# Optimization experiments

Hardware: AMD Instinct MI355X
Metric: run time of the kernel (lower is better)

Reference implementation:

```python
import jax, jax.numpy as jnp
import numpy as np

N_HEADS = 16
KQ_DIM = 64
EMB_DIM = 1024
CTX_DIM = 1024
EPS = 1e-5

def _layernorm(x, w, b):
    # LayerNorm over last dim (kq_dim), elementwise affine
    mu = jnp.mean(x, axis=-1, keepdims=True)
    var = jnp.mean(jnp.square(x - mu), axis=-1, keepdims=True)
    return (x - mu) * jax.lax.rsqrt(var + EPS) * w + b

def setup_inputs() -> dict:
    key = jax.random.key(0)
    ks = jax.random.split(key, 10)
    B, SQ, SK = 2, 2048, 2048
    inner = N_HEADS * KQ_DIM
    s_e = 1.0 / np.sqrt(EMB_DIM)
    s_c = 1.0 / np.sqrt(CTX_DIM)
    s_i = 1.0 / np.sqrt(inner)
    return {
        "emb": jax.random.normal(ks[0], (B, SQ, EMB_DIM), jnp.float32),
        "context": jax.random.normal(ks[1], (B, SK, CTX_DIM), jnp.float32),
        "Wq": jax.random.uniform(ks[2], (inner, EMB_DIM), jnp.float32, -s_e, s_e),
        "Wk": jax.random.uniform(ks[3], (inner, CTX_DIM), jnp.float32, -s_c, s_c),
        "Wv": jax.random.uniform(ks[4], (inner, CTX_DIM), jnp.float32, -s_c, s_c),
        "Wu": jax.random.uniform(ks[5], (EMB_DIM, inner), jnp.float32, -s_i, s_i),
        "bu": jax.random.uniform(ks[6], (EMB_DIM,), jnp.float32, -s_i, s_i),
        "qn_w": jnp.ones((KQ_DIM,), jnp.float32),
        "qn_b": jnp.zeros((KQ_DIM,), jnp.float32),
        "kn_w": jnp.ones((KQ_DIM,), jnp.float32),
        "kn_b": jnp.zeros((KQ_DIM,), jnp.float32),
    }

def reference(emb, context, Wq, Wk, Wv, Wu, bu, qn_w, qn_b, kn_w, kn_b):
    B, SQ, _ = emb.shape
    SK = context.shape[1]
    # projections (no bias), reshape to [B, H, S, D]
    q = (emb @ Wq.T).reshape(B, SQ, N_HEADS, KQ_DIM).transpose(0, 2, 1, 3)
    k = (context @ Wk.T).reshape(B, SK, N_HEADS, KQ_DIM).transpose(0, 2, 1, 3)
    v = (context @ Wv.T).reshape(B, SK, N_HEADS, KQ_DIM).transpose(0, 2, 1, 3)
    q = _layernorm(q, qn_w, qn_b)
    k = _layernorm(k, kn_w, kn_b)
    scale = 1.0 / jnp.sqrt(jnp.asarray(KQ_DIM, emb.dtype))
    attn = jnp.einsum('bhqd,bhkd->bhqk', q, k) * scale
    attn = jax.nn.softmax(attn, axis=-1)
    out = jnp.einsum('bhqk,bhkd->bhqd', attn, v)
    out = out.transpose(0, 2, 1, 3).reshape(B, SQ, N_HEADS * KQ_DIM)
    return out @ Wu.T + bu
```

## Files before the change

kernel.cpp:

```cpp
#include <hip/hip_runtime.h>


typedef __attribute__((ext_vector_type(8)))  short bf16x8;
typedef __attribute__((ext_vector_type(4)))  short bf16x4;
typedef __attribute__((ext_vector_type(4)))  float f32x4;
typedef __attribute__((ext_vector_type(16))) float f32x16;
typedef __attribute__((ext_vector_type(4)))  unsigned int u32x4;

#define SM_SCALE 0.18033688f

typedef __attribute__((address_space(1))) const void cg_void;
typedef __attribute__((address_space(3))) void lds_void_t;

__device__ __forceinline__ void gl_lds16(const void* g, void* l){
  __builtin_amdgcn_global_load_lds((cg_void*)g, (lds_void_t*)l, 16, 0, 0);
}

__device__ __forceinline__ short f2b(float f){
  unsigned int u;
  __builtin_memcpy(&u, &f, 4);
  u += 0x7fffu + ((u >> 16) & 1u);
  return (short)(u >> 16);
}

__global__ __launch_bounds__(256) void cvt6_kernel(
    const float* __restrict__ emb, const float* __restrict__ ctx,
    const float* __restrict__ Wq, const float* __restrict__ Wk,
    const float* __restrict__ Wv, const float* __restrict__ Wu,
    short* __restrict__ o_emb, short* __restrict__ o_ctx,
    short* __restrict__ o_wq, short* __restrict__ o_wk,
    short* __restrict__ o_wv, short* __restrict__ o_wu)
{
  const long M1 = 1024L * 1024L, M4 = 4L * M1;
  long e = ((long)blockIdx.x * 256 + threadIdx.x) * 4;
  if (e >= 12L * M1) return;
  const float* src; short* dst; long off;
  if      (e <     M4)      { src = emb; dst = o_emb; off = e;           }
  else if (e < 2 * M4)      { src = ctx; dst = o_ctx; off = e - M4;      }
  else if (e < 2 * M4 + M1) { src = Wq;  dst = o_wq;  off = e - 2 * M4;  }
  else if (e < 2 * M4 + 2*M1){src = Wk;  dst = o_wk;  off = e - 2*M4 - M1;}
  else if (e < 2 * M4 + 3*M1){src = Wv;  dst = o_wv;  off = e - 2*M4 - 2*M1;}
  else                      { src = Wu;  dst = o_wu;  off = e - 2*M4 - 3*M1;}
  f32x4 v = *(const f32x4*)(src + off);
  bf16x4 o;
  o[0] = f2b(v[0]); o[1] = f2b(v[1]); o[2] = f2b(v[2]); o[3] = f2b(v[3]);
  *(bf16x4*)(dst + off) = o;
}

__global__ __launch_bounds__(256, 3) void gemm_qkv_kernel(
    const short* __restrict__ embh, const short* __restrict__ ctxh,
    const short* __restrict__ Wqh, const short* __restrict__ Wkh,
    const short* __restrict__ Wvh,
    short* __restrict__ qo, short* __restrict__ ko, short* __restrict__ vto,
    const float* __restrict__ qw, const float* __restrict__ qb,
    const float* __restrict__ kw, const float* __restrict__ kb)
{
  const int K = 1024;
  __shared__ short As[128 * 64];
  __shared__ short Bs[128 * 64];
  const int tid  = threadIdx.x;
  const int wave = tid >> 6, lane = tid & 63;
  const int quad = lane >> 4, r16 = lane & 15;
  const int wm = (wave >> 1) * 64, wn = (wave & 1) * 64;

  const int task = blockIdx.y;
  int bn, bm;
  const short *A, *B;
  if (task == 2){
    bn = (blockIdx.x & 31) * 128; bm = (blockIdx.x >> 5) * 128;
    A = Wvh; B = ctxh;
  } else {
    bm = (blockIdx.x & 31) * 128; bn = (blockIdx.x >> 5) * 128;
    A = task ? ctxh : embh; B = task ? Wkh : Wqh;
  }

  f32x4 acc[4][4];
#pragma unroll
  for (int i = 0; i < 4; i++)
#pragma unroll
    for (int j = 0; j < 4; j++)
      acc[i][j] = (f32x4){0.f, 0.f, 0.f, 0.f};

  const int sr7 = (lane >> 3) & 7;
  const size_t arow = (size_t)(bm + wave * 8 + (lane >> 3)) * K
                      + (((lane & 7) ^ sr7) * 8);
  const size_t brow = (size_t)(bn + wave * 8 + (lane >> 3)) * K
                      + (((lane & 7) ^ sr7) * 8);
  const int sw = ((quad ^ (r16 & 7)) << 3);

  for (int k0 = 0; k0 < K; k0 += 64){
#pragma unroll
    for (int i = 0; i < 4; i++)
      gl_lds16(A + arow + (size_t)32 * i * K + k0, &As[wave * 512 + i * 2048]);
#pragma unroll
    for (int i = 0; i < 4; i++)
      gl_lds16(B + brow + (size_t)32 * i * K + k0, &Bs[wave * 512 + i * 2048]);
    __syncthreads();
#pragma unroll
    for (int kk = 0; kk < 2; kk++){
      const int off = sw ^ (kk << 5);
      bf16x8 af[4], bq[4];
#pragma unroll
      for (int i = 0; i < 4; i++)
        af[i] = *(const bf16x8*)(&As[(wm + i*16 + r16) * 64 + off]);
#pragma unroll
      for (int j = 0; j < 4; j++)
        bq[j] = *(const bf16x8*)(&Bs[(wn + j*16 + r16) * 64 + off]);
#pragma unroll
      for (int i = 0; i < 4; i++)
#pragma unroll
        for (int j = 0; j < 4; j++)
          acc[i][j] = __builtin_amdgcn_mfma_f32_16x16x32_bf16(af[i], bq[j], acc[i][j], 0, 0, 0);
    }
    __syncthreads();
  }

  if (task < 2){
    short* Ch = task ? ko : qo;
    const float* lw = task ? kw : qw;
    const float* lb = task ? kb : qb;
    const float post = task ? 1.0f : SM_SCALE;
    float wv[4], bv[4];
#pragma unroll
    for (int j = 0; j < 4; j++){
      wv[j] = lw[j*16 + r16] * post;
      bv[j] = lb[j*16 + r16] * post;
    }
#pragma unroll
    for (int i = 0; i < 4; i++){
#pragma unroll
      for (int t = 0; t < 4; t++){
        float a[4];
#pragma unroll
        for (int j = 0; j < 4; j++) a[j] = acc[i][j][t];
        float s = a[0] + a[1] + a[2] + a[3];
        s += __shfl_xor(s, 1); s += __shfl_xor(s, 2);
        s += __shfl_xor(s, 4); s += __shfl_xor(s, 8);
        const float mu = s * 0.015625f;
        float d[4], sq = 0.f;
#pragma unroll
        for (int j = 0; j < 4; j++){ d[j] = a[j] - mu; sq += d[j]*d[j]; }
        sq += __shfl_xor(sq, 1); sq += __shfl_xor(sq, 2);
        sq += __shfl_xor(sq, 4); sq += __shfl_xor(sq, 8);
        const float si = rsqrtf(sq * 0.015625f + 1e-5f);
        const size_t row = (size_t)(bm + wm + i*16 + quad*4 + t);
#pragma unroll
        for (int j = 0; j < 4; j++)
          Ch[row * 1024 + (bn + wn + j*16 + r16)] = f2b(d[j] * si * wv[j] + bv[j]);
      }
    }
  } else {
#pragma unroll
    for (int i = 0; i < 4; i++){
#pragma unroll
      for (int j4 = 0; j4 < 4; j4++){
#pragma unroll
        for (int t = 0; t < 4; t++){
          const int row  = bm + wm + i*16 + quad*4 + t;
          const int col0 = bn + wn + j4*16 + r16;
          const int bb  = col0 >> 11, tok = col0 & 2047;
          const int hq  = row >> 6,  dd  = row & 63;
          const int mt  = dd >> 5,   q5l = dd & 31;
          const int kt  = tok >> 6,  tk  = tok & 63;
          const int s32 = (tk >> 5) & 1, ks = tk & 31;
          const int hi  = ks >> 4,   r   = ks & 15;
          const int cc  = r >> 3, hh2 = (r >> 2) & 1, jj = (r & 3) + 4*hi;
          const size_t addr = ((size_t)(bb*16 + hq) * 32 + kt) * 4096
                            + (size_t)(((mt*2 + s32)*2 + cc) * 512)
                            + (hh2*32 + q5l) * 8 + jj;
          vto[addr] = f2b(acc[i][j4][t]);
        }
      }
    }
  }
}

__global__ __launch_bounds__(256, 4) void gemm_out_kernel(
    const short* __restrict__ A, const short* __restrict__ B,
    float* __restrict__ Cf, const float* __restrict__ bias)
{
  const int K = 1024, N = 1024;
  __shared__ short As[64 * 64];
  __shared__ short Bs[64 * 64];
  const int tid  = threadIdx.x;
  const int wave = tid >> 6, lane = tid & 63;
  const int quad = lane >> 4, r16 = lane & 15;
  const int wm = (wave >> 1) * 32, wn = (wave & 1) * 32;
  const int bm = blockIdx.x * 64, bn = blockIdx.y * 64;

  f32x4 acc[2][2];
#pragma unroll
  for (int i = 0; i < 2; i++)
#pragma unroll
    for (int j = 0; j < 2; j++)
      acc[i][j] = (f32x4){0.f, 0.f, 0.f, 0.f};

  const int sr7 = (lane >> 3) & 7;
  const size_t arow = (size_t)(bm + wave * 8 + (lane >> 3)) * K
                      + (((lane & 7) ^ sr7) * 8);
  const size_t brow = (size_t)(bn + wave * 8 + (lane >> 3)) * K
                      + (((lane & 7) ^ sr7) * 8);
  const int sw = ((quad ^ (r16 & 7)) << 3);

  for (int k0 = 0; k0 < K; k0 += 64){
#pragma unroll
    for (int i = 0; i < 2; i++){
      gl_lds16(A + arow + (size_t)32 * i * K + k0, &As[wave * 512 + i * 2048]);
      gl_lds16(B + brow + (size_t)32 * i * K + k0, &Bs[wave * 512 + i * 2048]);
    }
    __syncthreads();
#pragma unroll
    for (int kk = 0; kk < 2; kk++){
      const int off = sw ^ (kk << 5);
      bf16x8 af[2], bq[2];
#pragma unroll
      for (int i = 0; i < 2; i++)
        af[i] = *(const bf16x8*)(&As[(wm + i*16 + r16) * 64 + off]);
#pragma unroll
      for (int j = 0; j < 2; j++)
        bq[j] = *(const bf16x8*)(&Bs[(wn + j*16 + r16) * 64 + off]);
#pragma unroll
      for (int i = 0; i < 2; i++)
#pragma unroll
        for (int j = 0; j < 2; j++)
          acc[i][j] = __builtin_amdgcn_mfma_f32_16x16x32_bf16(af[i], bq[j], acc[i][j], 0, 0, 0);
    }
    __syncthreads();
  }

#pragma unroll
  for (int i = 0; i < 2; i++){
#pragma unroll
    for (int j = 0; j < 2; j++){
      const int col = bn + wn + j*16 + r16;
#pragma unroll
      for (int t = 0; t < 4; t++){
        const size_t row = (size_t)(bm + wm + i*16 + quad*4 + t);
        Cf[row * N + col] = acc[i][j][t] + bias[col];
      }
    }
  }
}

__global__ __launch_bounds__(256, 2) void flash2_kernel(
    const short* __restrict__ Q, const short* __restrict__ K,
    const short* __restrict__ Vt, short* __restrict__ O)
{
  __shared__ __align__(16) long long smem8[4096];
  short* Ks = (short*)smem8;
  float* scr = (float*)smem8;

  const int tid = threadIdx.x;
  const int wave = tid >> 6, lane = tid & 63;
  const int half = wave >> 1, wg = wave & 1;
  const int hh = lane >> 5, q5 = lane & 31;
  const int h = blockIdx.x, qb = blockIdx.y, b = blockIdx.z;
  const int q0 = qb * 128 + wg * 64;

  const size_t kbase = ((size_t)b * 2048) * 1024 + (size_t)h * 64;
  const short* vbh = Vt + ((size_t)(b * 16 + h)) * 131072;

  bf16x8 qf[2][4];
#pragma unroll
  for (int qg = 0; qg < 2; qg++){
    const size_t qrow = ((size_t)b * 2048 + q0 + qg * 32 + q5) * 1024 + (size_t)h * 64;
#pragma unroll
    for (int c = 0; c < 4; c++)
      qf[qg][c] = *(const bf16x8*)(Q + qrow + c * 16 + hh * 8);
  }

  f32x16 oacc[2][2];
#pragma unroll
  for (int t = 0; t < 16; t++){
    oacc[0][0][t] = 0.f; oacc[0][1][t] = 0.f;
    oacc[1][0][t] = 0.f; oacc[1][1][t] = 0.f;
  }
  float lacc[2] = {0.f, 0.f};

  const int srow = lane >> 3;
  const int csrc = ((lane & 7) ^ srow) * 8;
  const int wr0 = wg * 32;

#define STAGE(bufi, kt)                                                         \
  {                                                                             \
    const short* ks = K + kbase + (size_t)((kt) * 64 + wr0 + srow) * 1024 + csrc; \
    short* kd = Ks + (half * 2 + (bufi)) * 4096 + wr0 * 64;                     \
    gl_lds16(ks,             kd);                                               \
    gl_lds16(ks +  8 * 1024, kd + 512);                                         \
    gl_lds16(ks + 16 * 1024, kd + 1024);                                        \
    gl_lds16(ks + 24 * 1024, kd + 1536);                                        \
  }

  STAGE(0, half)

  for (int i = 0; i < 16; i++){
    const int buf = i & 1;
    __syncthreads();
    if (i + 1 < 16) STAGE(buf ^ 1, 2 * (i + 1) + half)

    const int ktc = 2 * i + half;

    bf16x8 vfr[2][2][2];
#pragma unroll
    for (int s32 = 0; s32 < 2; s32++)
#pragma unroll
      for (int c = 0; c < 2; c++)
#pragma unroll
        for (int mt = 0; mt < 2; mt++)
          vfr[s32][c][mt] = *(const bf16x8*)(
              vbh + (size_t)ktc * 4096 + (((mt*2 + s32)*2 + c) * 512) + lane * 8);

    const short* kb_l = Ks + (half * 2 + buf) * 4096;

    bf16x8 kf[2][4];
#pragma unroll
    for (int s32 = 0; s32 < 2; s32++){
      const int key = s32 * 32 + q5;
#pragma unroll
      for (int c = 0; c < 4; c++)
        kf[s32][c] = *(const bf16x8*)(&kb_l[key * 64 + (((2*c + hh) ^ (key & 7)) << 3)]);
    }

    f32x16 sacc[2][2];
#pragma unroll
    for (int t = 0; t < 16; t++){
      sacc[0][0][t] = 0.f; sacc[0][1][t] = 0.f;
      sacc[1][0][t] = 0.f; sacc[1][1][t] = 0.f;
    }
#pragma unroll
    for (int c = 0; c < 4; c++){
      sacc[0][0] = __builtin_amdgcn_mfma_f32_32x32x16_bf16(kf[0][c], qf[0][c], sacc[0][0], 0, 0, 0);
      sacc[0][1] = __builtin_amdgcn_mfma_f32_32x32x16_bf16(kf[1][c], qf[0][c], sacc[0][1], 0, 0, 0);
      sacc[1][0] = __builtin_amdgcn_mfma_f32_32x32x16_bf16(kf[0][c], qf[1][c], sacc[1][0], 0, 0, 0);
      sacc[1][1] = __builtin_amdgcn_mfma_f32_32x32x16_bf16(kf[1][c], qf[1][c], sacc[1][1], 0, 0, 0);
    }

    bf16x8 pf[2][2][2];
#pragma unroll
    for (int qg = 0; qg < 2; qg++){
#pragma unroll
      for (int s32 = 0; s32 < 2; s32++){
        unsigned int pu[16];
        float pp[4] = {0.f, 0.f, 0.f, 0.f};
#pragma unroll
        for (int t = 0; t < 16; t++){
          const float e = __builtin_amdgcn_exp2f(sacc[qg][s32][t]);
          pp[t & 3] += e;
          unsigned int u; __builtin_memcpy(&u, &e, 4);
          pu[t] = u + 0x8000u;
        }
        lacc[qg] += (pp[0] + pp[1]) + (pp[2] + pp[3]);
#pragma unroll
        for (int c = 0; c < 2; c++){
          u32x4 tmp;
          tmp[0] = __builtin_amdgcn_perm(pu[4*c + 1], pu[4*c + 0], 0x07060302u);
          tmp[1] = __builtin_amdgcn_perm(pu[4*c + 3], pu[4*c + 2], 0x07060302u);
          tmp[2] = __builtin_amdgcn_perm(pu[8 + 4*c + 1], pu[8 + 4*c + 0], 0x07060302u);
          tmp[3] = __builtin_amdgcn_perm(pu[8 + 4*c + 3], pu[8 + 4*c + 2], 0x07060302u);
          __builtin_memcpy(&pf[qg][s32][c], &tmp, 16);
        }
      }
    }

#pragma unroll
    for (int s32 = 0; s32 < 2; s32++){
#pragma unroll
      for (int c = 0; c < 2; c++){
#pragma unroll
        for (int mt = 0; mt < 2; mt++){
          oacc[0][mt] = __builtin_amdgcn_mfma_f32_32x32x16_bf16(vfr[s32][c][mt], pf[0][s32][c], oacc[0][mt], 0, 0, 0);
          oacc[1][mt] = __builtin_amdgcn_mfma_f32_32x32x16_bf16(vfr[s32][c][mt], pf[1][s32][c], oacc[1][mt], 0, 0, 0);
        }
      }
    }
  }

  const int widx = wg * 64 + lane;
  __syncthreads();
#pragma unroll
  for (int qg = 0; qg < 2; qg++){
    const float lh = lacc[qg] + __shfl_xor(lacc[qg], 32);
    if (half == 1){
      float* base = scr + widx * 33;
#pragma unroll
      for (int t = 0; t < 16; t++){ base[t] = oacc[qg][0][t]; base[16 + t] = oacc[qg][1][t]; }
      scr[4224 + widx] = lh;
    }
    __syncthreads();
    if (half == 0){
      const float* base = scr + widx * 33;
      const float l2 = scr[4224 + widx];
      const float linv = 1.0f / (lh + l2);
      const size_t orow = ((size_t)b * 2048 + q0 + qg * 32 + q5) * 1024 + (size_t)h * 64;
#pragma unroll
      for (int mt = 0; mt < 2; mt++){
#pragma unroll
        for (int g = 0; g < 4; g++){
          bf16x4 o4;
#pragma unroll
          for (int u = 0; u < 4; u++)
            o4[u] = f2b((oacc[qg][mt][g*4 + u] + base[mt*16 + g*4 + u]) * linv);
          *(bf16x4*)(O + orow + mt*32 + g*8 + 4*hh) = o4;
        }
      }
    }
    __syncthreads();
  }
}
#undef STAGE

extern "C" void kernel_launch(void* const* d_in, const int* in_sizes, int n_in,
                              void* d_out, int out_size, void* d_ws, size_t ws_size,
                              hipStream_t stream) {
  const float* emb  = (const float*)d_in[0];
  const float* ctx  = (const float*)d_in[1];
  const float* Wq   = (const float*)d_in[2];
  const float* Wk   = (const float*)d_in[3];
  const float* Wv   = (const float*)d_in[4];
  const float* Wu   = (const float*)d_in[5];
  const float* bu   = (const float*)d_in[6];
  const float* qn_w = (const float*)d_in[7];
  const float* qn_b = (const float*)d_in[8];
  const float* kn_w = (const float*)d_in[9];
  const float* kn_b = (const float*)d_in[10];
  float* out = (float*)d_out;

  const size_t BIG = (size_t)4096 * 1024;
  const size_t WSZ = (size_t)1024 * 1024;
  short* ws   = (short*)d_ws;
  short* embh = ws;
  short* ctxh = embh + BIG;
  short* Wqh  = ctxh + BIG;
  short* Wkh  = Wqh + WSZ;
  short* Wvh  = Wkh + WSZ;
  short* Wuh  = Wvh + WSZ;
  short* qh   = Wuh + WSZ;
  short* kh   = qh + BIG;
  short* vth  = kh + BIG;
  short* aoh  = vth + BIG;

  cvt6_kernel<<<12288, 256, 0, stream>>>(emb, ctx, Wq, Wk, Wv, Wu,
                                         embh, ctxh, Wqh, Wkh, Wvh, Wuh);

  gemm_qkv_kernel<<<dim3(256, 3), 256, 0, stream>>>(
      embh, ctxh, Wqh, Wkh, Wvh, qh, kh, vth,
      qn_w, qn_b, kn_w, kn_b);

  flash2_kernel<<<dim3(16, 16, 2), 256, 0, stream>>>(qh, kh, vth, aoh);

  gemm_out_kernel<<<dim3(64, 16), 256, 0, stream>>>(aoh, Wuh, out, bu);
}
```

Baseline: 190.4 us.

## Pre-swizzle K into MFMA fragment layout and load directly to registers

```diff
diff --git a/kernel.cpp b/kernel.cpp
--- a/kernel.cpp
+++ b/kernel.cpp
@@ -116,7 +116,6 @@
   }
 
   if (task < 2){
-    short* Ch = task ? ko : qo;
     const float* lw = task ? kw : qw;
     const float* lb = task ? kb : qb;
     const float post = task ? 1.0f : SM_SCALE;
@@ -143,10 +142,27 @@
         sq += __shfl_xor(sq, 1); sq += __shfl_xor(sq, 2);
         sq += __shfl_xor(sq, 4); sq += __shfl_xor(sq, 8);
         const float si = rsqrtf(sq * 0.015625f + 1e-5f);
-        const size_t row = (size_t)(bm + wm + i*16 + quad*4 + t);
-#pragma unroll
-        for (int j = 0; j < 4; j++)
-          Ch[row * 1024 + (bn + wn + j*16 + r16)] = f2b(d[j] * si * wv[j] + bv[j]);
+        const int row = bm + wm + i*16 + quad*4 + t;
+        if (task == 0){
+#pragma unroll
+          for (int j = 0; j < 4; j++)
+            qo[(size_t)row * 1024 + (bn + wn + j*16 + r16)] =
+                f2b(d[j] * si * wv[j] + bv[j]);
+        } else {
+          const int bb = row >> 11, key = row & 2047;
+          const int kt = key >> 6, tk = key & 63;
+          const int s32 = tk >> 5, q5k = tk & 31;
+#pragma unroll
+          for (int j = 0; j < 4; j++){
+            const int col = bn + wn + j*16 + r16;
+            const int hq = col >> 6, dd = col & 63;
+            const int cc = dd >> 4, hh2 = (dd >> 3) & 1, jj = dd & 7;
+            const size_t addr = ((size_t)(bb*16 + hq) * 32 + kt) * 4096
+                              + (size_t)((s32*4 + cc) * 512)
+                              + (hh2*32 + q5k) * 8 + jj;
+            ko[addr] = f2b(d[j] * si * wv[j] + bv[j]);
+          }
+        }
       }
     }
   } else {
@@ -243,12 +259,10 @@
 }
 
 __global__ __launch_bounds__(256, 2) void flash2_kernel(
-    const short* __restrict__ Q, const short* __restrict__ K,
+    const short* __restrict__ Q, const short* __restrict__ Kf,
     const short* __restrict__ Vt, short* __restrict__ O)
 {
-  __shared__ __align__(16) long long smem8[4096];
-  short* Ks = (short*)smem8;
-  float* scr = (float*)smem8;
+  __shared__ __align__(16) float scr[4352];
 
   const int tid = threadIdx.x;
   const int wave = tid >> 6, lane = tid & 63;
@@ -257,7 +271,7 @@
   const int h = blockIdx.x, qb = blockIdx.y, b = blockIdx.z;
   const int q0 = qb * 128 + wg * 64;
 
-  const size_t kbase = ((size_t)b * 2048) * 1024 + (size_t)h * 64;
+  const short* kbh = Kf + ((size_t)(b * 16 + h)) * 131072;
   const short* vbh = Vt + ((size_t)(b * 16 + h)) * 131072;
 
   bf16x8 qf[2][4];
@@ -277,103 +291,91 @@
   }
   float lacc[2] = {0.f, 0.f};
 
-  const int srow = lane >> 3;
-  const int csrc = ((lane & 7) ^ srow) * 8;
-  const int wr0 = wg * 32;
-
-#define STAGE(bufi, kt)                                                         \
-  {                                                                             \
-    const short* ks = K + kbase + (size_t)((kt) * 64 + wr0 + srow) * 1024 + csrc; \
-    short* kd = Ks + (half * 2 + (bufi)) * 4096 + wr0 * 64;                     \
-    gl_lds16(ks,             kd);                                               \
-    gl_lds16(ks +  8 * 1024, kd + 512);                                         \
-    gl_lds16(ks + 16 * 1024, kd + 1024);                                        \
-    gl_lds16(ks + 24 * 1024, kd + 1536);                                        \
-  }
-
-  STAGE(0, half)
-
-  for (int i = 0; i < 16; i++){
-    const int buf = i & 1;
-    __syncthreads();
-    if (i + 1 < 16) STAGE(buf ^ 1, 2 * (i + 1) + half)
-
-    const int ktc = 2 * i + half;
-
-    bf16x8 vfr[2][2][2];
-#pragma unroll
-    for (int s32 = 0; s32 < 2; s32++)
-#pragma unroll
-      for (int c = 0; c < 2; c++)
-#pragma unroll
-        for (int mt = 0; mt < 2; mt++)
-          vfr[s32][c][mt] = *(const bf16x8*)(
-              vbh + (size_t)ktc * 4096 + (((mt*2 + s32)*2 + c) * 512) + lane * 8);
-
-    const short* kb_l = Ks + (half * 2 + buf) * 4096;
-
-    bf16x8 kf[2][4];
-#pragma unroll
-    for (int s32 = 0; s32 < 2; s32++){
-      const int key = s32 * 32 + q5;
-#pragma unroll
-      for (int c = 0; c < 4; c++)
-        kf[s32][c] = *(const bf16x8*)(&kb_l[key * 64 + (((2*c + hh) ^ (key & 7)) << 3)]);
-    }
-
-    f32x16 sacc[2][2];
-#pragma unroll
-    for (int t = 0; t < 16; t++){
-      sacc[0][0][t] = 0.f; sacc[0][1][t] = 0.f;
-      sacc[1][0][t] = 0.f; sacc[1][1][t] = 0.f;
-    }
-#pragma unroll
-    for (int c = 0; c < 4; c++){
-      sacc[0][0] = __builtin_amdgcn_mfma_f32_32x32x16_bf16(kf[0][c], qf[0][c], sacc[0][0], 0, 0, 0);
-      sacc[0][1] = __builtin_amdgcn_mfma_f32_32x32x16_bf16(kf[1][c], qf[0][c], sacc[0][1], 0, 0, 0);
-      sacc[1][0] = __builtin_amdgcn_mfma_f32_32x32x16_bf16(kf[0][c], qf[1][c], sacc[1][0], 0, 0, 0);
-      sacc[1][1] = __builtin_amdgcn_mfma_f32_32x32x16_bf16(kf[1][c], qf[1][c], sacc[1][1], 0, 0, 0);
-    }
-
-    bf16x8 pf[2][2][2];
-#pragma unroll
-    for (int qg = 0; qg < 2; qg++){
-#pragma unroll
-      for (int s32 = 0; s32 < 2; s32++){
-        unsigned int pu[16];
-        float pp[4] = {0.f, 0.f, 0.f, 0.f};
-#pragma unroll
-        for (int t = 0; t < 16; t++){
-          const float e = __builtin_amdgcn_exp2f(sacc[qg][s32][t]);
-          pp[t & 3] += e;
-          unsigned int u; __builtin_memcpy(&u, &e, 4);
-          pu[t] = u + 0x8000u;
-        }
-        lacc[qg] += (pp[0] + pp[1]) + (pp[2] + pp[3]);
-#pragma unroll
-        for (int c = 0; c < 2; c++){
-          u32x4 tmp;
-          tmp[0] = __builtin_amdgcn_perm(pu[4*c + 1], pu[4*c + 0], 0x07060302u);
-          tmp[1] = __builtin_amdgcn_perm(pu[4*c + 3], pu[4*c + 2], 0x07060302u);
-          tmp[2] = __builtin_amdgcn_perm(pu[8 + 4*c + 1], pu[8 + 4*c + 0], 0x07060302u);
-          tmp[3] = __builtin_amdgcn_perm(pu[8 + 4*c + 3], pu[8 + 4*c + 2], 0x07060302u);
-          __builtin_memcpy(&pf[qg][s32][c], &tmp, 16);
-        }
-      }
-    }
-
-#pragma unroll
-    for (int s32 = 0; s32 < 2; s32++){
-#pragma unroll
-      for (int c = 0; c < 2; c++){
-#pragma unroll
-        for (int mt = 0; mt < 2; mt++){
-          oacc[0][mt] = __builtin_amdgcn_mfma_f32_32x32x16_bf16(vfr[s32][c][mt], pf[0][s32][c], oacc[0][mt], 0, 0, 0);
-          oacc[1][mt] = __builtin_amdgcn_mfma_f32_32x32x16_bf16(vfr[s32][c][mt], pf[1][s32][c], oacc[1][mt], 0, 0, 0);
-        }
-      }
-    }
-  }
+#define LOADK(dst, ktc)                                                      \
+  {                                                                          \
+    const short* kp = kbh + (size_t)(ktc) * 4096 + lane * 8;                 \
+    _Pragma("unroll")                                                        \
+    for (int s32 = 0; s32 < 2; s32++)                                        \
+      _Pragma("unroll")                                                      \
+      for (int c = 0; c < 4; c++)                                            \
+        dst[s32][c] = *(const bf16x8*)(kp + (s32*4 + c) * 512);              \
+  }
+
+#define BODY(kfX, ktc)                                                       \
+  {                                                                          \
+    bf16x8 vfr[2][2][2];                                                     \
+    _Pragma("unroll")                                                        \
+    for (int s32 = 0; s32 < 2; s32++)                                        \
+      _Pragma("unroll")                                                      \
+      for (int c = 0; c < 2; c++)                                            \
+        _Pragma("unroll")                                                    \
+        for (int mt = 0; mt < 2; mt++)                                       \
+          vfr[s32][c][mt] = *(const bf16x8*)(                                \
+              vbh + (size_t)(ktc) * 4096 + (((mt*2 + s32)*2 + c) * 512) + lane * 8); \
+    f32x16 sacc[2][2];                                                       \
+    _Pragma("unroll")                                                        \
+    for (int t = 0; t < 16; t++){                                            \
+      sacc[0][0][t] = 0.f; sacc[0][1][t] = 0.f;                              \
+      sacc[1][0][t] = 0.f; sacc[1][1][t] = 0.f;                              \
+    }                                                                        \
+    _Pragma("unroll")                                                        \
+    for (int c = 0; c < 4; c++){                                             \
+      sacc[0][0] = __builtin_amdgcn_mfma_f32_32x32x16_bf16(kfX[0][c], qf[0][c], sacc[0][0], 0, 0, 0); \
+      sacc[0][1] = __builtin_amdgcn_mfma_f32_32x32x16_bf16(kfX[1][c], qf[0][c], sacc[0][1], 0, 0, 0); \
+      sacc[1][0] = __builtin_amdgcn_mfma_f32_32x32x16_bf16(kfX[0][c], qf[1][c], sacc[1][0], 0, 0, 0); \
+      sacc[1][1] = __builtin_amdgcn_mfma_f32_32x32x16_bf16(kfX[1][c], qf[1][c], sacc[1][1], 0, 0, 0); \
+    }                                                                        \
+    bf16x8 pf[2][2][2];                                                      \
+    _Pragma("unroll")                                                        \
+    for (int qg = 0; qg < 2; qg++){                                          \
+      _Pragma("unroll")                                                      \
+      for (int s32 = 0; s32 < 2; s32++){                                     \
+        unsigned int pu[16];                                                 \
+        float pp[4] = {0.f, 0.f, 0.f, 0.f};                                  \
+        _Pragma("unroll")                                                    \
+        for (int t = 0; t < 16; t++){                                        \
+          const float e = __builtin_amdgcn_exp2f(sacc[qg][s32][t]);          \
+          pp[t & 3] += e;                                                    \
+          unsigned int u; __builtin_memcpy(&u, &e, 4);                       \
+          pu[t] = u + 0x8000u;                                               \
+        }                                                                    \
+        lacc[qg] += (pp[0] + pp[1]) + (pp[2] + pp[3]);                       \
+        _Pragma("unroll")                                                    \
+        for (int c = 0; c < 2; c++){                                         \
+          u32x4 tmp;                                                         \
+          tmp[0] = __builtin_amdgcn_perm(pu[4*c + 1], pu[4*c + 0], 0x07060302u); \
+          tmp[1] = __builtin_amdgcn_perm(pu[4*c + 3], pu[4*c + 2], 0x07060302u); \
+          tmp[2] = __builtin_amdgcn_perm(pu[8 + 4*c + 1], pu[8 + 4*c + 0], 0x07060302u); \
+          tmp[3] = __builtin_amdgcn_perm(pu[8 + 4*c + 3], pu[8 + 4*c + 2], 0x07060302u); \
+          __builtin_memcpy(&pf[qg][s32][c], &tmp, 16);                       \
+        }                                                                    \
+      }                                                                      \
+    }                                                                        \
+    _Pragma("unroll")                                                        \
+    for (int s32 = 0; s32 < 2; s32++){                                       \
+      _Pragma("unroll")                                                      \
+      for (int c = 0; c < 2; c++){                                           \
+        _Pragma("unroll")                                                    \
+        for (int mt = 0; mt < 2; mt++){                                      \
+          oacc[0][mt] = __builtin_amdgcn_mfma_f32_32x32x16_bf16(vfr[s32][c][mt], pf[0][s32][c], oacc[0][mt], 0, 0, 0); \
+          oacc[1][mt] = __builtin_amdgcn_mfma_f32_32x32x16_bf16(vfr[s32][c][mt], pf[1][s32][c], oacc[1][mt], 0, 0, 0); \
+        }                                                                    \
+      }                                                                      \
+    }                                                                        \
+  }
+
+  bf16x8 kfA[2][4], kfB[2][4];
+  LOADK(kfA, half)
+
+  for (int t = 0; t < 16; t += 2){
+    const int kt0 = 2 * t + half;
+    LOADK(kfB, kt0 + 2)
+    BODY(kfA, kt0)
+    if (t + 2 < 16) LOADK(kfA, kt0 + 4)
+    BODY(kfB, kt0 + 2)
+  }
+#undef LOADK
+#undef BODY
 
   const int widx = wg * 64 + lane;
   __syncthreads();
@@ -407,7 +409,6 @@
     __syncthreads();
   }
 }
-#undef STAGE
 
 extern "C" void kernel_launch(void* const* d_in, const int* in_sizes, int n_in,
                               void* d_out, int out_size, void* d_ws, size_t ws_size,
```

New measurement: 202.5 us. +6.4%, slower.

## Store K in MFMA fragment layout and load K fragments directly from global

Applied to the files above, without the earlier changes.

```diff
diff --git a/kernel.cpp b/kernel.cpp
--- a/kernel.cpp
+++ b/kernel.cpp
@@ -116,7 +116,6 @@
   }
 
   if (task < 2){
-    short* Ch = task ? ko : qo;
     const float* lw = task ? kw : qw;
     const float* lb = task ? kb : qb;
     const float post = task ? 1.0f : SM_SCALE;
@@ -143,10 +142,27 @@
         sq += __shfl_xor(sq, 1); sq += __shfl_xor(sq, 2);
         sq += __shfl_xor(sq, 4); sq += __shfl_xor(sq, 8);
         const float si = rsqrtf(sq * 0.015625f + 1e-5f);
-        const size_t row = (size_t)(bm + wm + i*16 + quad*4 + t);
-#pragma unroll
-        for (int j = 0; j < 4; j++)
-          Ch[row * 1024 + (bn + wn + j*16 + r16)] = f2b(d[j] * si * wv[j] + bv[j]);
+        const int row = bm + wm + i*16 + quad*4 + t;
+        if (task == 0){
+#pragma unroll
+          for (int j = 0; j < 4; j++)
+            qo[(size_t)row * 1024 + (bn + wn + j*16 + r16)] =
+                f2b(d[j] * si * wv[j] + bv[j]);
+        } else {
+          const int bb = row >> 11, key = row & 2047;
+          const int kt = key >> 6, tk = key & 63;
+          const int s32 = tk >> 5, q5k = tk & 31;
+#pragma unroll
+          for (int j = 0; j < 4; j++){
+            const int col = bn + wn + j*16 + r16;
+            const int hq = col >> 6, dd = col & 63;
+            const int cc = dd >> 4, hh2 = (dd >> 3) & 1, jj = dd & 7;
+            const size_t addr = ((size_t)(bb*16 + hq) * 32 + kt) * 4096
+                              + (size_t)((s32*4 + cc) * 512)
+                              + (hh2*32 + q5k) * 8 + jj;
+            ko[addr] = f2b(d[j] * si * wv[j] + bv[j]);
+          }
+        }
       }
     }
   } else {
@@ -243,12 +259,10 @@
 }
 
 __global__ __launch_bounds__(256, 2) void flash2_kernel(
-    const short* __restrict__ Q, const short* __restrict__ K,
+    const short* __restrict__ Q, const short* __restrict__ Kf,
     const short* __restrict__ Vt, short* __restrict__ O)
 {
-  __shared__ __align__(16) long long smem8[4096];
-  short* Ks = (short*)smem8;
-  float* scr = (float*)smem8;
+  __shared__ __align__(16) float scr[4352];
 
   const int tid = threadIdx.x;
   const int wave = tid >> 6, lane = tid & 63;
@@ -257,7 +271,7 @@
   const int h = blockIdx.x, qb = blockIdx.y, b = blockIdx.z;
   const int q0 = qb * 128 + wg * 64;
 
-  const size_t kbase = ((size_t)b * 2048) * 1024 + (size_t)h * 64;
+  const short* kbh = Kf + ((size_t)(b * 16 + h)) * 131072;
   const short* vbh = Vt + ((size_t)(b * 16 + h)) * 131072;
 
   bf16x8 qf[2][4];
@@ -277,49 +291,17 @@
   }
   float lacc[2] = {0.f, 0.f};
 
-  const int srow = lane >> 3;
-  const int csrc = ((lane & 7) ^ srow) * 8;
-  const int wr0 = wg * 32;
-
-#define STAGE(bufi, kt)                                                         \
-  {                                                                             \
-    const short* ks = K + kbase + (size_t)((kt) * 64 + wr0 + srow) * 1024 + csrc; \
-    short* kd = Ks + (half * 2 + (bufi)) * 4096 + wr0 * 64;                     \
-    gl_lds16(ks,             kd);                                               \
-    gl_lds16(ks +  8 * 1024, kd + 512);                                         \
-    gl_lds16(ks + 16 * 1024, kd + 1024);                                        \
-    gl_lds16(ks + 24 * 1024, kd + 1536);                                        \
-  }
-
-  STAGE(0, half)
-
   for (int i = 0; i < 16; i++){
-    const int buf = i & 1;
-    __syncthreads();
-    if (i + 1 < 16) STAGE(buf ^ 1, 2 * (i + 1) + half)
-
     const int ktc = 2 * i + half;
-
-    bf16x8 vfr[2][2][2];
+    const short* kp = kbh + (size_t)ktc * 4096 + lane * 8;
+    const short* vp = vbh + (size_t)ktc * 4096 + lane * 8;
+
+    bf16x8 kf[2][4];
 #pragma unroll
     for (int s32 = 0; s32 < 2; s32++)
 #pragma unroll
-      for (int c = 0; c < 2; c++)
-#pragma unroll
-        for (int mt = 0; mt < 2; mt++)
-          vfr[s32][c][mt] = *(const bf16x8*)(
-              vbh + (size_t)ktc * 4096 + (((mt*2 + s32)*2 + c) * 512) + lane * 8);
-
-    const short* kb_l = Ks + (half * 2 + buf) * 4096;
-
-    bf16x8 kf[2][4];
-#pragma unroll
-    for (int s32 = 0; s32 < 2; s32++){
-      const int key = s32 * 32 + q5;
-#pragma unroll
       for (int c = 0; c < 4; c++)
-        kf[s32][c] = *(const bf16x8*)(&kb_l[key * 64 + (((2*c + hh) ^ (key & 7)) << 3)]);
-    }
+        kf[s32][c] = *(const bf16x8*)(kp + (s32*4 + c) * 512);
 
     f32x16 sacc[2][2];
 #pragma unroll
@@ -334,6 +316,15 @@
       sacc[1][0] = __builtin_amdgcn_mfma_f32_32x32x16_bf16(kf[0][c], qf[1][c], sacc[1][0], 0, 0, 0);
       sacc[1][1] = __builtin_amdgcn_mfma_f32_32x32x16_bf16(kf[1][c], qf[1][c], sacc[1][1], 0, 0, 0);
     }
+
+    bf16x8 vfr[2][2][2];
+#pragma unroll
+    for (int s32 = 0; s32 < 2; s32++)
+#pragma unroll
+      for (int c = 0; c < 2; c++)
+#pragma unroll
+        for (int mt = 0; mt < 2; mt++)
+          vfr[s32][c][mt] = *(const bf16x8*)(vp + (((mt*2 + s32)*2 + c) * 512));
 
     bf16x8 pf[2][2][2];
 #pragma unroll
@@ -407,7 +398,6 @@
     __syncthreads();
   }
 }
-#undef STAGE
 
 extern "C" void kernel_launch(void* const* d_in, const int* in_sizes, int n_in,
                               void* d_out, int out_size, void* d_ws, size_t ws_size,
```

Measured after the change: 194.8 us. 2.3% more time.
